# Optimization experiments

Measured on AMD Instinct MI355X. Metric: run time of the kernel, lower is better.

## Reference

```python
import jax, jax.numpy as jnp
import numpy as np

# iRPE config: ratio=1.9, method='euc', mode='ctx', shared_head=True, skip=1, rpe_on='k'
ALPHA, BETA, GAMMA = 1.9, 3.8, 15.2  # alpha=1*ratio, beta=2*ratio, gamma=8*ratio
NUM_HEADS = 12


def _rp_bucket_euc(height, width, skip):
    """Static relative-position bucket ids (Euclidean method, piecewise index).
    Returns (skip+L, skip+L) int array and num_buckets."""
    coords = np.stack(np.meshgrid(np.arange(height), np.arange(width), indexing='ij'), -1)
    coords = coords.reshape(-1, 2).astype(np.float64)  # (L, 2)
    diff = coords[:, None, :] - coords[None, :, :]      # (L, L, 2)
    dis = np.round(np.sqrt((diff ** 2).sum(-1)))        # (L, L), nonnegative
    # piecewise_index: identity for dis<=alpha, log-spaced (rounded, clipped at beta) beyond
    log_idx = np.minimum(
        np.round(ALPHA + np.log(np.maximum(dis, 1e-9) / ALPHA) / np.log(GAMMA / ALPHA) * (BETA - ALPHA)),
        BETA).astype(np.int64)
    bucket = np.where(dis <= ALPHA, np.round(dis).astype(np.int64), log_idx)
    bucket = bucket - bucket.min()
    nb = 2 * int(BETA) + 1  # 7
    if skip > 0:
        L = height * width
        full = np.full((skip + L, skip + L), nb, dtype=np.int64)  # extra bucket for cls token
        full[skip:, skip:] = bucket
        bucket, nb = full, nb + 1  # nb = 8
    return jnp.asarray(bucket), nb


def setup_inputs() -> dict:
    key = jax.random.key(0)
    ks = jax.random.split(key, 4)
    B, N, C = 8, 1025, 768  # 32x32 patches + 1 cls token
    hd = C // NUM_HEADS
    nb = 2 * int(BETA) + 1 + 1  # 8 buckets (incl. skip bucket)
    return {
        "x": jax.random.normal(ks[0], (B, N, C), jnp.float32),
        "qkv_w": jax.random.normal(ks[1], (3 * C, C), jnp.float32) * 0.02,
        "proj_w": jax.random.normal(ks[2], (C, C), jnp.float32) * 0.02,
        "proj_b": jnp.zeros((C,), jnp.float32),
        "rpe_w": jax.random.normal(ks[3], (hd, nb), jnp.float32) * 0.02,  # shared across heads
    }


def reference(x, qkv_w, proj_w, proj_b, rpe_w):
    B, N, C = x.shape
    H = NUM_HEADS
    hd = C // H
    scale = hd ** -0.5
    n_modalities = 1
    height = int((N // n_modalities) ** 0.5)        # 32 (mask is None path)
    skip = N - n_modalities * height * height       # 1 (cls token)
    rp_bucket, _ = _rp_bucket_euc(height, height, skip)  # (N, N) int, static

    qkv = (x @ qkv_w.T).reshape(B, N, 3, H, hd).transpose(2, 0, 3, 1, 4)  # (3,B,H,N,hd)
    q, k, v = qkv[0] * scale, qkv[1], qkv[2]
    attn = jnp.einsum('bhid,bhjd->bhij', q, k)
    # contextual RPE on keys (shared head): bias[b,h,i,j] = q[b,h,i,:] @ rpe_w[:, bucket[i,j]]
    lookup = jnp.einsum('bhid,dm->bhim', q, rpe_w)                      # (B,H,N,nb)
    bias = jnp.take_along_axis(lookup, rp_bucket[None, None, :, :], axis=3)  # (B,H,N,N)
    attn = jax.nn.softmax(attn + bias, axis=-1)
    out = jnp.einsum('bhij,bhjd->bhid', attn, v)
    out = out.transpose(0, 2, 1, 3).reshape(B, N, C)
    return out @ proj_w.T + proj_b
```

## Files before the change

kernel.cpp:

```cpp
#include <hip/hip_runtime.h>
#include <math.h>

#define B_    8
#define N_    1025
#define H_    12
#define HD_   64
#define C_    768
#define BH_   (B_*H_)
#define NTOK  (B_*N_)
#define SCALE 0.125f
#define NPAD  1092
#define NPADV 1088

#define QKV_ELEMS (BH_*N_*HD_)

#define XB_OFF_B     ((size_t)0)
#define WQKV_OFF_B   (XB_OFF_B + (size_t)NTOK*C_*2)
#define WPROJ_OFF_B  (WQKV_OFF_B + (size_t)3*C_*C_*2)
#define QB_OFF_B     (WPROJ_OFF_B + (size_t)C_*C_*2)
#define KB_OFF_B     (QB_OFF_B + (size_t)QKV_ELEMS*2)
#define AOB_OFF_B    (KB_OFF_B + (size_t)QKV_ELEMS*2)
#define VT_OFF_B     (AOB_OFF_B + (size_t)QKV_ELEMS*2)
#define BUCKET_OFF_B (VT_OFF_B + (size_t)BH_*HD_*NPADV*2)

typedef __attribute__((ext_vector_type(8))) short s8bf;
typedef __attribute__((ext_vector_type(8))) unsigned short u8s;
typedef __attribute__((ext_vector_type(4))) float v4f;
typedef unsigned short ushort_t;

#define GLOAD16(gp, lp) __builtin_amdgcn_global_load_lds( \
    (const __attribute__((address_space(1))) unsigned int*)(gp), \
    (__attribute__((address_space(3))) unsigned int*)(lp), 16, 0, 0)

#define SBAR() do { \
    __builtin_amdgcn_sched_barrier(0); \
    asm volatile("s_barrier" ::: "memory"); \
    __builtin_amdgcn_sched_barrier(0); \
} while (0)
#define VMW(N) do { \
    __builtin_amdgcn_sched_barrier(0); \
    asm volatile("s_waitcnt vmcnt(" #N ")" ::: "memory"); \
    __builtin_amdgcn_sched_barrier(0); \
} while (0)

__device__ __forceinline__ unsigned short f2bf(float x) {
    union { float f; unsigned u; } v; v.f = x;
    unsigned r = v.u + 0x7FFFu + ((v.u >> 16) & 1u);
    return (unsigned short)(r >> 16);
}
__device__ __forceinline__ unsigned packbf_hu(float lo, float hi) {
    union { float f; unsigned u; } a, b; a.f = lo; b.f = hi;
    return ((a.u + 0x8000u) >> 16) | ((b.u + 0x8000u) & 0xFFFF0000u);
}

__global__ void bucket_kernel(unsigned char* __restrict__ bucketT) {
    int tid = blockIdx.x * 256 + threadIdx.x;
    if (tid >= N_ * NPAD) return;
    unsigned ut = (unsigned)tid;
    int j = ut / (unsigned)NPAD, i = ut % (unsigned)NPAD;
    if (i >= N_) i = N_ - 1;
    int bk;
    if (i < 1 || j < 1) {
        bk = 7;
    } else {
        int pi = i - 1, pj = j - 1;
        int dy = (pi >> 5) - (pj >> 5);
        int dx = (pi & 31) - (pj & 31);
        int d2 = dy*dy + dx*dx;
        bk = (d2 == 0) ? 0 : ((d2 <= 2) ? 1 : ((d2 <= 12) ? 2 : 3));
    }
    bucketT[tid] = (unsigned char)bk;
}

__global__ __launch_bounds__(256) void cast_kernel(
        const float* __restrict__ x, const float* __restrict__ w1,
        const float* __restrict__ w2,
        ushort_t* __restrict__ xb, ushort_t* __restrict__ w1b,
        ushort_t* __restrict__ w2b) {
    const int NX = NTOK * C_ / 8, NW1 = 3 * C_ * C_ / 8, NW2 = C_ * C_ / 8;
    int g = blockIdx.x * 256 + threadIdx.x;
    const float* src; ushort_t* dst; int idx;
    if (g < NX)                 { src = x;  dst = xb;  idx = g; }
    else if (g < NX + NW1)      { src = w1; dst = w1b; idx = g - NX; }
    else if (g < NX + NW1 + NW2){ src = w2; dst = w2b; idx = g - NX - NW1; }
    else return;
    size_t off = (size_t)idx * 8;
    float4 a = *(const float4*)(src + off);
    float4 c = *(const float4*)(src + off + 4);
    __align__(16) ushort_t h[8] = {f2bf(a.x), f2bf(a.y), f2bf(a.z), f2bf(a.w),
                                   f2bf(c.x), f2bf(c.y), f2bf(c.z), f2bf(c.w)};
    *(u8s*)(dst + off) = *(u8s*)h;
}

__global__ __launch_bounds__(256) void qkv_kernel(
        const ushort_t* __restrict__ xb, const ushort_t* __restrict__ wb,
        ushort_t* __restrict__ qb, ushort_t* __restrict__ kb, ushort_t* __restrict__ vt) {
    __shared__ __align__(16) ushort_t As0[128*64];
    __shared__ __align__(16) ushort_t Bs0[128*64];
    __shared__ __align__(16) ushort_t As1[128*64];
    __shared__ __align__(16) ushort_t Bs1[128*64];
    const int L = blockIdx.x + blockIdx.y * 65;
    const int xcd = L & 7, idx = L >> 3;
    const int wg = (xcd < 2 ? xcd * 147 : 2 * 147 + (xcd - 2) * 146) + idx;
    const int m0 = (wg / 18) * 128, c0 = (wg % 18) * 128;
    const int t = threadIdx.x;
    const int w = t >> 6, lane = t & 63, lc = lane & 15, lq = lane >> 4;
    const int wm = (w >> 1) * 64, wn = (w & 1) * 64;
    const int srow8 = w * 32 + (lane >> 3);
    const int gsw8  = (((lane & 7) ^ (lane >> 3)) & 7) * 8;

    v4f acc[4][4];
#pragma unroll
    for (int mt = 0; mt < 4; mt++)
#pragma unroll
        for (int nt = 0; nt < 4; nt++) acc[mt][nt] = (v4f){0.f, 0.f, 0.f, 0.f};

    auto STAGE = [&](ushort_t* Ad, ushort_t* Bd, int k0) {
#pragma unroll
        for (int i = 0; i < 4; i++) {
            int row = srow8 + i * 8;
            int m = m0 + row; if (m > NTOK - 1) m = NTOK - 1;
            GLOAD16(xb + (size_t)m * C_ + k0 + gsw8,           &Ad[(w*32 + i*8) * 64]);
            GLOAD16(wb + (size_t)(c0 + row) * C_ + k0 + gsw8,  &Bd[(w*32 + i*8) * 64]);
        }
    };
    auto COMPUTE = [&](const ushort_t* A, const ushort_t* B) {
#pragma unroll
        for (int kk = 0; kk < 64; kk += 32) {
            s8bf af[4], bf[4];
#pragma unroll
            for (int mt = 0; mt < 4; mt++)
                af[mt] = *(const s8bf*)&A[(wm + mt*16 + lc) * 64 + ((((kk>>3) + lq) ^ (lc & 7)) * 8)];
#pragma unroll
            for (int nt = 0; nt < 4; nt++)
                bf[nt] = *(const s8bf*)&B[(wn + nt*16 + lc) * 64 + ((((kk>>3) + lq) ^ (lc & 7)) * 8)];
#pragma unroll
            for (int mt = 0; mt < 4; mt++)
#pragma unroll
                for (int nt = 0; nt < 4; nt++)
                    acc[mt][nt] = __builtin_amdgcn_mfma_f32_16x16x32_bf16(af[mt], bf[nt], acc[mt][nt], 0, 0, 0);
        }
    };

    STAGE(As0, Bs0, 0);
#pragma unroll
    for (int it = 0; it < 6; ++it) {
        const int k0 = it * 128;
        if (k0 + 64 < C_) {
            STAGE(As1, Bs1, k0 + 64);
            asm volatile("s_waitcnt vmcnt(8)" ::: "memory");
        } else {
            asm volatile("s_waitcnt vmcnt(0)" ::: "memory");
        }
        SBAR();
        COMPUTE(As0, Bs0);
        SBAR();
        if (k0 + 128 < C_) {
            STAGE(As0, Bs0, k0 + 128);
            asm volatile("s_waitcnt vmcnt(8)" ::: "memory");
        } else {
            asm volatile("s_waitcnt vmcnt(0)" ::: "memory");
        }
        SBAR();
        COMPUTE(As1, Bs1);
        if (it < 5) SBAR();
    }

#pragma unroll
    for (int mt = 0; mt < 4; mt++) {
#pragma unroll
        for (int r = 0; r < 4; r++) {
            int m = m0 + wm + mt*16 + lq*4 + r;
            if (m >= NTOK) continue;
            unsigned um = (unsigned)m;
            int b = um / (unsigned)N_, n = um % (unsigned)N_;
#pragma unroll
            for (int nt = 0; nt < 4; nt++) {
                int c = c0 + wn + nt*16 + lc;
                int comp = c / C_, rem = c % C_;
                int h = rem >> 6, d0 = rem & 63;
                float val = acc[mt][nt][r] * ((comp == 0) ? SCALE : 1.0f);
                if (comp == 2) {
                    vt[((size_t)((b*H_ + h)*HD_ + d0))*NPADV + n] = f2bf(val);
                } else {
                    ushort_t* dst = (comp == 0) ? qb : kb;
                    dst[((size_t)((b*H_ + h)*N_ + n))*HD_ + d0] = f2bf(val);
                }
            }
        }
    }
}

#define LUTS 9

__global__ __launch_bounds__(256) void attn_kernel(
        const ushort_t* __restrict__ qb, const ushort_t* __restrict__ kb,
        const ushort_t* __restrict__ vt, const float* __restrict__ rpe,
        const unsigned char* __restrict__ bucketT, ushort_t* __restrict__ ao) {
    __shared__ __align__(16) ushort_t Ks0[64*64];
    __shared__ __align__(16) ushort_t Vs0[64*64];
    __shared__ __align__(16) ushort_t Ks1[64*64];
    __shared__ __align__(16) ushort_t Vs1[64*64];
    __shared__ float lut[64*LUTS];

    const int bh = blockIdx.x, it0 = blockIdx.y;
    const int b  = bh / H_, hh = bh % H_;
    const int i0 = it0 * 64;
    const int t  = threadIdx.x;
    const int w  = t >> 6, lane = t & 63, lc = lane & 15, lq = lane >> 4;
    const int row_w = w * 16;
    const int rs = lc & 7;
    const int gA = ((lq ^ rs) & 7) * 8;
    const int gB = (((lq + 4) ^ rs) & 7) * 8;

    const ushort_t* qp = qb + (size_t)bh * N_ * HD_;
    const ushort_t* kp = kb + (size_t)bh * N_ * HD_;
    const ushort_t* vp = vt + (size_t)bh * HD_ * NPADV;

    {
        int row = t >> 2, g0 = (t & 3) * 2, qrs = row & 7;
        int gi = i0 + row;
        u8s h0 = (u8s)0, h1 = (u8s)0;
        if (gi < N_) {
            h0 = *(const u8s*)(qp + (size_t)gi * HD_ + g0*8);
            h1 = *(const u8s*)(qp + (size_t)gi * HD_ + g0*8 + 8);
        }
        *(u8s*)&Vs1[row*64 + ((g0 ^ qrs) * 8)]       = h0;
        *(u8s*)&Vs1[row*64 + (((g0+1) ^ qrs) * 8)]   = h1;
    }
    if (t < 64) {
        float4 r0 = *(const float4*)(rpe + t*8);
        float4 r1 = *(const float4*)(rpe + t*8 + 4);
        const int gr = t >> 3, go = t & 7;
        float vals[8] = {r0.x, r0.y, r0.z, r0.w, r1.x, r1.y, r1.z, r1.w};
#pragma unroll
        for (int m = 0; m < 8; m++)
            Ks1[m*64 + ((gr ^ (m & 7)) * 8) + go] = f2bf(vals[m]);
    } else if (t < 128) {
        int idx = t - 64;
        int m = 8 + (idx >> 3), g = idx & 7;
        *(u8s*)&Ks1[m*64 + ((g ^ (m & 7)) * 8)] = (u8s)0;
    }
    __syncthreads();

    s8bf qf0 = *(s8bf*)&Vs1[(row_w + lc)*64 + gA];
    s8bf qf1 = *(s8bf*)&Vs1[(row_w + lc)*64 + gB];

    {
        s8bf rf0 = *(s8bf*)&Ks1[lc*64 + gA];
        s8bf rf1 = *(s8bf*)&Ks1[lc*64 + gB];
        v4f la = (v4f){0.f, 0.f, 0.f, 0.f};
        la = __builtin_amdgcn_mfma_f32_16x16x32_bf16(qf0, rf0, la, 0, 0, 0);
        la = __builtin_amdgcn_mfma_f32_16x16x32_bf16(qf1, rf1, la, 0, 0, 0);
        if (lc < 8) {
#pragma unroll
            for (int r = 0; r < 4; r++)
                lut[(row_w + lq*4 + r)*LUTS + lc] = la[r];
        }
    }

    int myrow = i0 + row_w + lc; if (myrow > N_ - 1) myrow = N_ - 1;
    const unsigned char* bkrow = bucketT + (size_t)myrow * NPAD;
    const int lutbase = (row_w + lc) * LUTS;
    const int jb0 = 8*lq, jb1 = 8*lq + 4, jb2 = 8*lq + 32, jb3 = 8*lq + 36;
    unsigned bk4[4];

    auto STAGEA = [&](ushort_t* Kd, ushort_t* Vd, int jbase) {
#pragma unroll
        for (int i = 0; i < 2; i++) {
            int s = w*16 + i*8 + (lane >> 3);
            int jr = 32*(s>>5) + 8*((s>>2)&3) + 4*((s>>4)&1) + (s&3);
            int gj = jbase + jr; if (gj > N_ - 1) gj = N_ - 1;
            GLOAD16(kp + (size_t)gj * HD_ + (((lane&7) ^ (s&7)) * 8), &Kd[(w*16 + i*8)*64]);
        }
#pragma unroll
        for (int i = 0; i < 2; i++) {
            int d = w*16 + i*8 + (lane >> 3);
            GLOAD16(vp + (size_t)d * NPADV + jbase + (((lane&7) ^ (d&7)) * 8), &Vd[(w*16 + i*8)*64]);
        }
    };

    v4f o[4];
    float lsum = 0.f;
#pragma unroll
    for (int dt = 0; dt < 4; dt++) o[dt] = (v4f){0.f, 0.f, 0.f, 0.f};

    auto TILE = [&](const ushort_t* Kb, const ushort_t* Vb, int nextj, bool tail) {
        v4f acc[4];
#pragma unroll
        for (int t4 = 0; t4 < 4; t4++) acc[t4] = (v4f){0.f, 0.f, 0.f, 0.f};
#pragma unroll
        for (int t4 = 0; t4 < 4; t4++) {
            s8bf kf0 = *(const s8bf*)&Kb[(t4*16 + lc)*64 + gA];
            s8bf kf1 = *(const s8bf*)&Kb[(t4*16 + lc)*64 + gB];
            acc[t4] = __builtin_amdgcn_mfma_f32_16x16x32_bf16(kf0, qf0, acc[t4], 0, 0, 0);
            acc[t4] = __builtin_amdgcn_mfma_f32_16x16x32_bf16(kf1, qf1, acc[t4], 0, 0, 0);
        }
        unsigned pw[8];
        if (!tail) {
#pragma unroll
            for (int t4 = 0; t4 < 4; t4++) {
                int k0b = (bk4[t4]      ) & 0xFF; float p0 = __expf(acc[t4][0] + lut[lutbase + k0b]);
                int k1b = (bk4[t4] >>  8) & 0xFF; float p1 = __expf(acc[t4][1] + lut[lutbase + k1b]);
                int k2b = (bk4[t4] >> 16) & 0xFF; float p2 = __expf(acc[t4][2] + lut[lutbase + k2b]);
                int k3b = (bk4[t4] >> 24)       ; float p3 = __expf(acc[t4][3] + lut[lutbase + k3b]);
                lsum += (p0 + p1) + (p2 + p3);
                pw[t4*2]     = packbf_hu(p0, p1);
                pw[t4*2 + 1] = packbf_hu(p2, p3);
            }
        } else {
            const int jbs[4] = {jb0, jb1, jb2, jb3};
#pragma unroll
            for (int t4 = 0; t4 < 4; t4++) {
                float pv[4];
#pragma unroll
                for (int r = 0; r < 4; r++) {
                    int bk = (bk4[t4] >> (8*r)) & 0xFF;
                    float p = __expf(acc[t4][r] + lut[lutbase + bk]);
                    if ((jbs[t4] + r) > 0) p = 0.f;
                    lsum += p;
                    pv[r] = p;
                }
                pw[t4*2]     = packbf_hu(pv[0], pv[1]);
                pw[t4*2 + 1] = packbf_hu(pv[2], pv[3]);
            }
        }
        if (nextj >= 0) {
            bk4[0] = *(const unsigned*)(bkrow + nextj + jb0);
            bk4[1] = *(const unsigned*)(bkrow + nextj + jb1);
            bk4[2] = *(const unsigned*)(bkrow + nextj + jb2);
            bk4[3] = *(const unsigned*)(bkrow + nextj + jb3);
        }
        s8bf pf0 = *(s8bf*)&pw[0];
        s8bf pf1 = *(s8bf*)&pw[4];
#pragma unroll
        for (int dt = 0; dt < 4; dt++) {
            s8bf vf0 = *(const s8bf*)&Vb[(dt*16 + lc)*64 + gA];
            s8bf vf1 = *(const s8bf*)&Vb[(dt*16 + lc)*64 + gB];
            o[dt] = __builtin_amdgcn_mfma_f32_16x16x32_bf16(pf0, vf0, o[dt], 0, 0, 0);
            o[dt] = __builtin_amdgcn_mfma_f32_16x16x32_bf16(pf1, vf1, o[dt], 0, 0, 0);
        }
    };

    STAGEA(Ks0, Vs0, 0);
    bk4[0] = *(const unsigned*)(bkrow + jb0);
    bk4[1] = *(const unsigned*)(bkrow + jb1);
    bk4[2] = *(const unsigned*)(bkrow + jb2);
    bk4[3] = *(const unsigned*)(bkrow + jb3);
    SBAR();

    for (int it = 0; it < 8; ++it) {
        const int j0 = it * 128;
        STAGEA(Ks1, Vs1, j0 + 64);
        VMW(4);
        SBAR();
        TILE(Ks0, Vs0, j0 + 64, false);
        SBAR();
        STAGEA(Ks0, Vs0, j0 + 128);
        VMW(4);
        SBAR();
        TILE(Ks1, Vs1, j0 + 128, false);
        SBAR();
    }
    VMW(0);
    SBAR();
    TILE(Ks0, Vs0, -1, true);

    lsum += __shfl_xor(lsum, 16);
    lsum += __shfl_xor(lsum, 32);
    if (lq == 0) lut[(row_w + lc)*LUTS + 8] = lsum;
    __builtin_amdgcn_s_waitcnt(0);
#pragma unroll
    for (int r = 0; r < 4; r++) {
        int i = i0 + row_w + lq*4 + r;
        if (i < N_) {
            float inv = 1.0f / lut[(row_w + lq*4 + r)*LUTS + 8];
#pragma unroll
            for (int dt = 0; dt < 4; dt++)
                ao[((size_t)(b*N_ + i))*C_ + hh*HD_ + dt*16 + lc] = f2bf(o[dt][r] * inv);
        }
    }
}

__global__ __launch_bounds__(256) void proj_kernel(
        const ushort_t* __restrict__ ab, const ushort_t* __restrict__ wb,
        const float* __restrict__ bias, float* __restrict__ out) {
    __shared__ __align__(16) ushort_t As0[128*64];
    __shared__ __align__(16) ushort_t Bs0[128*64];
    __shared__ __align__(16) ushort_t As1[128*64];
    __shared__ __align__(16) ushort_t Bs1[128*64];
    const int L = blockIdx.x + blockIdx.y * 65;
    const int xcd = L & 7, idx = L >> 3;
    const int wg = (xcd < 6 ? xcd * 49 : 6 * 49 + (xcd - 6) * 48) + idx;
    const int m0 = (wg / 6) * 128, c0 = (wg % 6) * 128;
    const int t = threadIdx.x;
    const int w = t >> 6, lane = t & 63, lc = lane & 15, lq = lane >> 4;
    const int wm = (w >> 1) * 64, wn = (w & 1) * 64;
    const int srow8 = w * 32 + (lane >> 3);
    const int gsw8  = (((lane & 7) ^ (lane >> 3)) & 7) * 8;

    v4f acc[4][4];
#pragma unroll
    for (int mt = 0; mt < 4; mt++)
#pragma unroll
        for (int nt = 0; nt < 4; nt++) acc[mt][nt] = (v4f){0.f, 0.f, 0.f, 0.f};

    auto STAGE = [&](ushort_t* Ad, ushort_t* Bd, int k0) {
#pragma unroll
        for (int i = 0; i < 4; i++) {
            int row = srow8 + i * 8;
            int m = m0 + row; if (m > NTOK - 1) m = NTOK - 1;
            GLOAD16(ab + (size_t)m * C_ + k0 + gsw8,           &Ad[(w*32 + i*8) * 64]);
            GLOAD16(wb + (size_t)(c0 + row) * C_ + k0 + gsw8,  &Bd[(w*32 + i*8) * 64]);
        }
    };
    auto COMPUTE = [&](const ushort_t* A, const ushort_t* B) {
#pragma unroll
        for (int kk = 0; kk < 64; kk += 32) {
            s8bf af[4], bf[4];
#pragma unroll
            for (int mt = 0; mt < 4; mt++)
                af[mt] = *(const s8bf*)&A[(wm + mt*16 + lc) * 64 + ((((kk>>3) + lq) ^ (lc & 7)) * 8)];
#pragma unroll
            for (int nt = 0; nt < 4; nt++)
                bf[nt] = *(const s8bf*)&B[(wn + nt*16 + lc) * 64 + ((((kk>>3) + lq) ^ (lc & 7)) * 8)];
#pragma unroll
            for (int mt = 0; mt < 4; mt++)
#pragma unroll
                for (int nt = 0; nt < 4; nt++)
                    acc[mt][nt] = __builtin_amdgcn_mfma_f32_16x16x32_bf16(af[mt], bf[nt], acc[mt][nt], 0, 0, 0);
        }
    };

    STAGE(As0, Bs0, 0);
#pragma unroll
    for (int it = 0; it < 6; ++it) {
        const int k0 = it * 128;
        if (k0 + 64 < C_) {
            STAGE(As1, Bs1, k0 + 64);
            asm volatile("s_waitcnt vmcnt(8)" ::: "memory");
        } else {
            asm volatile("s_waitcnt vmcnt(0)" ::: "memory");
        }
        SBAR();
        COMPUTE(As0, Bs0);
        SBAR();
        if (k0 + 128 < C_) {
            STAGE(As0, Bs0, k0 + 128);
            asm volatile("s_waitcnt vmcnt(8)" ::: "memory");
        } else {
            asm volatile("s_waitcnt vmcnt(0)" ::: "memory");
        }
        SBAR();
        COMPUTE(As1, Bs1);
        if (it < 5) SBAR();
    }

    float pb[4];
#pragma unroll
    for (int nt = 0; nt < 4; nt++) pb[nt] = bias[c0 + wn + nt*16 + lc];
#pragma unroll
    for (int mt = 0; mt < 4; mt++) {
#pragma unroll
        for (int r = 0; r < 4; r++) {
            int m = m0 + wm + mt*16 + lq*4 + r;
            if (m >= NTOK) continue;
#pragma unroll
            for (int nt = 0; nt < 4; nt++) {
                int c = c0 + wn + nt*16 + lc;
                out[(size_t)m * C_ + c] = acc[mt][nt][r] + pb[nt];
            }
        }
    }
}

extern "C" void kernel_launch(void* const* d_in, const int* in_sizes, int n_in,
                              void* d_out, int out_size, void* d_ws, size_t ws_size,
                              hipStream_t stream) {
    const float* x      = (const float*)d_in[0];
    const float* qkv_w  = (const float*)d_in[1];
    const float* proj_w = (const float*)d_in[2];
    const float* proj_b = (const float*)d_in[3];
    const float* rpe_w  = (const float*)d_in[4];
    float* out = (float*)d_out;

    char* ws = (char*)d_ws;
    ushort_t* xb   = (ushort_t*)(ws + XB_OFF_B);
    ushort_t* wqkv = (ushort_t*)(ws + WQKV_OFF_B);
    ushort_t* wprj = (ushort_t*)(ws + WPROJ_OFF_B);
    ushort_t* qb   = (ushort_t*)(ws + QB_OFF_B);
    ushort_t* kb   = (ushort_t*)(ws + KB_OFF_B);
    ushort_t* aob  = (ushort_t*)(ws + AOB_OFF_B);
    ushort_t* vt   = (ushort_t*)(ws + VT_OFF_B);
    unsigned char* bucketT = (unsigned char*)(ws + BUCKET_OFF_B);

    const int ncast = (NTOK*C_ + 3*C_*C_ + C_*C_) / 8;
    bucket_kernel<<<dim3((N_*NPAD + 255)/256), 256, 0, stream>>>(bucketT);
    cast_kernel<<<dim3((ncast + 255)/256), 256, 0, stream>>>(x, qkv_w, proj_w, xb, wqkv, wprj);
    qkv_kernel<<<dim3(65, 18), 256, 0, stream>>>(xb, wqkv, qb, kb, vt);
    attn_kernel<<<dim3(96, 17), 256, 0, stream>>>(qb, kb, vt, rpe_w, bucketT, aob);
    proj_kernel<<<dim3(65, 6), 256, 0, stream>>>(aob, wprj, proj_b, out);
}
```

Before: 232.1 us.

## Process two 64-row query tiles per attention block to reuse K/V tiles

```diff
diff --git a/kernel.cpp b/kernel.cpp
--- a/kernel.cpp
+++ b/kernel.cpp
@@ -201,11 +201,11 @@
     __shared__ __align__(16) ushort_t Vs0[64*64];
     __shared__ __align__(16) ushort_t Ks1[64*64];
     __shared__ __align__(16) ushort_t Vs1[64*64];
-    __shared__ float lut[64*LUTS];
+    __shared__ float lut[128*LUTS];
 
     const int bh = blockIdx.x, it0 = blockIdx.y;
     const int b  = bh / H_, hh = bh % H_;
-    const int i0 = it0 * 64;
+    const int i0 = it0 * 128;
     const int t  = threadIdx.x;
     const int w  = t >> 6, lane = t & 63, lc = lane & 15, lq = lane >> 4;
     const int row_w = w * 16;
@@ -243,27 +243,48 @@
     }
     __syncthreads();
 
-    s8bf qf0 = *(s8bf*)&Vs1[(row_w + lc)*64 + gA];
-    s8bf qf1 = *(s8bf*)&Vs1[(row_w + lc)*64 + gB];
+    s8bf qfa0 = *(s8bf*)&Vs1[(row_w + lc)*64 + gA];
+    s8bf qfa1 = *(s8bf*)&Vs1[(row_w + lc)*64 + gB];
+    s8bf rf0 = *(s8bf*)&Ks1[lc*64 + gA];
+    s8bf rf1 = *(s8bf*)&Ks1[lc*64 + gB];
+    v4f la_a = (v4f){0.f, 0.f, 0.f, 0.f};
+    la_a = __builtin_amdgcn_mfma_f32_16x16x32_bf16(qfa0, rf0, la_a, 0, 0, 0);
+    la_a = __builtin_amdgcn_mfma_f32_16x16x32_bf16(qfa1, rf1, la_a, 0, 0, 0);
+    __syncthreads();
 
     {
-        s8bf rf0 = *(s8bf*)&Ks1[lc*64 + gA];
-        s8bf rf1 = *(s8bf*)&Ks1[lc*64 + gB];
-        v4f la = (v4f){0.f, 0.f, 0.f, 0.f};
-        la = __builtin_amdgcn_mfma_f32_16x16x32_bf16(qf0, rf0, la, 0, 0, 0);
-        la = __builtin_amdgcn_mfma_f32_16x16x32_bf16(qf1, rf1, la, 0, 0, 0);
-        if (lc < 8) {
-#pragma unroll
-            for (int r = 0; r < 4; r++)
-                lut[(row_w + lq*4 + r)*LUTS + lc] = la[r];
-        }
-    }
-
-    int myrow = i0 + row_w + lc; if (myrow > N_ - 1) myrow = N_ - 1;
-    const unsigned char* bkrow = bucketT + (size_t)myrow * NPAD;
-    const int lutbase = (row_w + lc) * LUTS;
+        int row = t >> 2, g0 = (t & 3) * 2, qrs = row & 7;
+        int gi = i0 + 64 + row;
+        u8s h0 = (u8s)0, h1 = (u8s)0;
+        if (gi < N_) {
+            h0 = *(const u8s*)(qp + (size_t)gi * HD_ + g0*8);
+            h1 = *(const u8s*)(qp + (size_t)gi * HD_ + g0*8 + 8);
+        }
+        *(u8s*)&Vs1[row*64 + ((g0 ^ qrs) * 8)]       = h0;
+        *(u8s*)&Vs1[row*64 + (((g0+1) ^ qrs) * 8)]   = h1;
+    }
+    __syncthreads();
+    s8bf qfb0 = *(s8bf*)&Vs1[(row_w + lc)*64 + gA];
+    s8bf qfb1 = *(s8bf*)&Vs1[(row_w + lc)*64 + gB];
+    v4f la_b = (v4f){0.f, 0.f, 0.f, 0.f};
+    la_b = __builtin_amdgcn_mfma_f32_16x16x32_bf16(qfb0, rf0, la_b, 0, 0, 0);
+    la_b = __builtin_amdgcn_mfma_f32_16x16x32_bf16(qfb1, rf1, la_b, 0, 0, 0);
+    if (lc < 8) {
+#pragma unroll
+        for (int r = 0; r < 4; r++) {
+            lut[(row_w + lq*4 + r)*LUTS + lc]        = la_a[r];
+            lut[(64 + row_w + lq*4 + r)*LUTS + lc]   = la_b[r];
+        }
+    }
+
+    int myrow_a = i0 + row_w + lc;       if (myrow_a > N_ - 1) myrow_a = N_ - 1;
+    int myrow_b = i0 + 64 + row_w + lc;  if (myrow_b > N_ - 1) myrow_b = N_ - 1;
+    const unsigned char* bkrow_a = bucketT + (size_t)myrow_a * NPAD;
+    const unsigned char* bkrow_b = bucketT + (size_t)myrow_b * NPAD;
+    const int lutbase_a = (row_w + lc) * LUTS;
+    const int lutbase_b = (64 + row_w + lc) * LUTS;
     const int jb0 = 8*lq, jb1 = 8*lq + 4, jb2 = 8*lq + 32, jb3 = 8*lq + 36;
-    unsigned bk4[4];
+    unsigned bka[4], bkb[4];
 
     auto STAGEA = [&](ushort_t* Kd, ushort_t* Vd, int jbase) {
 #pragma unroll
@@ -280,73 +301,101 @@
         }
     };
 
-    v4f o[4];
-    float lsum = 0.f;
-#pragma unroll
-    for (int dt = 0; dt < 4; dt++) o[dt] = (v4f){0.f, 0.f, 0.f, 0.f};
+    v4f oa[4], ob[4];
+    float lsa = 0.f, lsb = 0.f;
+#pragma unroll
+    for (int dt = 0; dt < 4; dt++) { oa[dt] = (v4f){0.f,0.f,0.f,0.f}; ob[dt] = (v4f){0.f,0.f,0.f,0.f}; }
 
     auto TILE = [&](const ushort_t* Kb, const ushort_t* Vb, int nextj, bool tail) {
-        v4f acc[4];
-#pragma unroll
-        for (int t4 = 0; t4 < 4; t4++) acc[t4] = (v4f){0.f, 0.f, 0.f, 0.f};
+        v4f aa[4], ab[4];
+#pragma unroll
+        for (int t4 = 0; t4 < 4; t4++) { aa[t4] = (v4f){0.f,0.f,0.f,0.f}; ab[t4] = (v4f){0.f,0.f,0.f,0.f}; }
 #pragma unroll
         for (int t4 = 0; t4 < 4; t4++) {
             s8bf kf0 = *(const s8bf*)&Kb[(t4*16 + lc)*64 + gA];
             s8bf kf1 = *(const s8bf*)&Kb[(t4*16 + lc)*64 + gB];
-            acc[t4] = __builtin_amdgcn_mfma_f32_16x16x32_bf16(kf0, qf0, acc[t4], 0, 0, 0);
-            acc[t4] = __builtin_amdgcn_mfma_f32_16x16x32_bf16(kf1, qf1, acc[t4], 0, 0, 0);
-        }
-        unsigned pw[8];
+            aa[t4] = __builtin_amdgcn_mfma_f32_16x16x32_bf16(kf0, qfa0, aa[t4], 0, 0, 0);
+            aa[t4] = __builtin_amdgcn_mfma_f32_16x16x32_bf16(kf1, qfa1, aa[t4], 0, 0, 0);
+            ab[t4] = __builtin_amdgcn_mfma_f32_16x16x32_bf16(kf0, qfb0, ab[t4], 0, 0, 0);
+            ab[t4] = __builtin_amdgcn_mfma_f32_16x16x32_bf16(kf1, qfb1, ab[t4], 0, 0, 0);
+        }
+        unsigned pwa[8], pwb[8];
         if (!tail) {
 #pragma unroll
             for (int t4 = 0; t4 < 4; t4++) {
-                int k0b = (bk4[t4]      ) & 0xFF; float p0 = __expf(acc[t4][0] + lut[lutbase + k0b]);
-                int k1b = (bk4[t4] >>  8) & 0xFF; float p1 = __expf(acc[t4][1] + lut[lutbase + k1b]);
-                int k2b = (bk4[t4] >> 16) & 0xFF; float p2 = __expf(acc[t4][2] + lut[lutbase + k2b]);
-                int k3b = (bk4[t4] >> 24)       ; float p3 = __expf(acc[t4][3] + lut[lutbase + k3b]);
-                lsum += (p0 + p1) + (p2 + p3);
-                pw[t4*2]     = packbf_hu(p0, p1);
-                pw[t4*2 + 1] = packbf_hu(p2, p3);
+                int k0b = (bka[t4]      ) & 0xFF; float p0 = __expf(aa[t4][0] + lut[lutbase_a + k0b]);
+                int k1b = (bka[t4] >>  8) & 0xFF; float p1 = __expf(aa[t4][1] + lut[lutbase_a + k1b]);
+                int k2b = (bka[t4] >> 16) & 0xFF; float p2 = __expf(aa[t4][2] + lut[lutbase_a + k2b]);
+                int k3b = (bka[t4] >> 24)       ; float p3 = __expf(aa[t4][3] + lut[lutbase_a + k3b]);
+                lsa += (p0 + p1) + (p2 + p3);
+                pwa[t4*2]     = packbf_hu(p0, p1);
+                pwa[t4*2 + 1] = packbf_hu(p2, p3);
+            }
+#pragma unroll
+            for (int t4 = 0; t4 < 4; t4++) {
+                int k0b = (bkb[t4]      ) & 0xFF; float p0 = __expf(ab[t4][0] + lut[lutbase_b + k0b]);
+                int k1b = (bkb[t4] >>  8) & 0xFF; float p1 = __expf(ab[t4][1] + lut[lutbase_b + k1b]);
+                int k2b = (bkb[t4] >> 16) & 0xFF; float p2 = __expf(ab[t4][2] + lut[lutbase_b + k2b]);
+                int k3b = (bkb[t4] >> 24)       ; float p3 = __expf(ab[t4][3] + lut[lutbase_b + k3b]);
+                lsb += (p0 + p1) + (p2 + p3);
+                pwb[t4*2]     = packbf_hu(p0, p1);
+                pwb[t4*2 + 1] = packbf_hu(p2, p3);
             }
         } else {
             const int jbs[4] = {jb0, jb1, jb2, jb3};
 #pragma unroll
             for (int t4 = 0; t4 < 4; t4++) {
-                float pv[4];
+                float pva[4], pvb[4];
 #pragma unroll
                 for (int r = 0; r < 4; r++) {
-                    int bk = (bk4[t4] >> (8*r)) & 0xFF;
-                    float p = __expf(acc[t4][r] + lut[lutbase + bk]);
-                    if ((jbs[t4] + r) > 0) p = 0.f;
-                    lsum += p;
-                    pv[r] = p;
+                    bool jv = (jbs[t4] + r) == 0;
+                    int bk_a = (bka[t4] >> (8*r)) & 0xFF;
+                    float pa = __expf(aa[t4][r] + lut[lutbase_a + bk_a]);
+                    if (!jv) pa = 0.f;
+                    lsa += pa; pva[r] = pa;
+                    int bk_b = (bkb[t4] >> (8*r)) & 0xFF;
+                    float pb2 = __expf(ab[t4][r] + lut[lutbase_b + bk_b]);
+                    if (!jv) pb2 = 0.f;
+                    lsb += pb2; pvb[r] = pb2;
                 }
-                pw[t4*2]     = packbf_hu(pv[0], pv[1]);
-                pw[t4*2 + 1] = packbf_hu(pv[2], pv[3]);
+                pwa[t4*2] = packbf_hu(pva[0], pva[1]); pwa[t4*2+1] = packbf_hu(pva[2], pva[3]);
+                pwb[t4*2] = packbf_hu(pvb[0], pvb[1]); pwb[t4*2+1] = packbf_hu(pvb[2], pvb[3]);
             }
         }
         if (nextj >= 0) {
-            bk4[0] = *(const unsigned*)(bkrow + nextj + jb0);
-            bk4[1] = *(const unsigned*)(bkrow + nextj + jb1);
-            bk4[2] = *(const unsigned*)(bkrow + nextj + jb2);
-            bk4[3] = *(const unsigned*)(bkrow + nextj + jb3);
-        }
-        s8bf pf0 = *(s8bf*)&pw[0];
-        s8bf pf1 = *(s8bf*)&pw[4];
+            bka[0] = *(const unsigned*)(bkrow_a + nextj + jb0);
+            bka[1] = *(const unsigned*)(bkrow_a + nextj + jb1);
+            bka[2] = *(const unsigned*)(bkrow_a + nextj + jb2);
+            bka[3] = *(const unsigned*)(bkrow_a + nextj + jb3);
+            bkb[0] = *(const unsigned*)(bkrow_b + nextj + jb0);
+            bkb[1] = *(const unsigned*)(bkrow_b + nextj + jb1);
+            bkb[2] = *(const unsigned*)(bkrow_b + nextj + jb2);
+            bkb[3] = *(const unsigned*)(bkrow_b + nextj + jb3);
+        }
+        s8bf pfa0 = *(s8bf*)&pwa[0];
+        s8bf pfa1 = *(s8bf*)&pwa[4];
+        s8bf pfb0 = *(s8bf*)&pwb[0];
+        s8bf pfb1 = *(s8bf*)&pwb[4];
 #pragma unroll
         for (int dt = 0; dt < 4; dt++) {
             s8bf vf0 = *(const s8bf*)&Vb[(dt*16 + lc)*64 + gA];
             s8bf vf1 = *(const s8bf*)&Vb[(dt*16 + lc)*64 + gB];
-            o[dt] = __builtin_amdgcn_mfma_f32_16x16x32_bf16(pf0, vf0, o[dt], 0, 0, 0);
-            o[dt] = __builtin_amdgcn_mfma_f32_16x16x32_bf16(pf1, vf1, o[dt], 0, 0, 0);
+            oa[dt] = __builtin_amdgcn_mfma_f32_16x16x32_bf16(pfa0, vf0, oa[dt], 0, 0, 0);
+            oa[dt] = __builtin_amdgcn_mfma_f32_16x16x32_bf16(pfa1, vf1, oa[dt], 0, 0, 0);
+            ob[dt] = __builtin_amdgcn_mfma_f32_16x16x32_bf16(pfb0, vf0, ob[dt], 0, 0, 0);
+            ob[dt] = __builtin_amdgcn_mfma_f32_16x16x32_bf16(pfb1, vf1, ob[dt], 0, 0, 0);
         }
     };
 
     STAGEA(Ks0, Vs0, 0);
-    bk4[0] = *(const unsigned*)(bkrow + jb0);
-    bk4[1] = *(const unsigned*)(bkrow + jb1);
-    bk4[2] = *(const unsigned*)(bkrow + jb2);
-    bk4[3] = *(const unsigned*)(bkrow + jb3);
+    bka[0] = *(const unsigned*)(bkrow_a + jb0);
+    bka[1] = *(const unsigned*)(bkrow_a + jb1);
+    bka[2] = *(const unsigned*)(bkrow_a + jb2);
+    bka[3] = *(const unsigned*)(bkrow_a + jb3);
+    bkb[0] = *(const unsigned*)(bkrow_b + jb0);
+    bkb[1] = *(const unsigned*)(bkrow_b + jb1);
+    bkb[2] = *(const unsigned*)(bkrow_b + jb2);
+    bkb[3] = *(const unsigned*)(bkrow_b + jb3);
     SBAR();
 
     for (int it = 0; it < 8; ++it) {
@@ -366,9 +415,14 @@
     SBAR();
     TILE(Ks0, Vs0, -1, true);
 
-    lsum += __shfl_xor(lsum, 16);
-    lsum += __shfl_xor(lsum, 32);
-    if (lq == 0) lut[(row_w + lc)*LUTS + 8] = lsum;
+    lsa += __shfl_xor(lsa, 16);
+    lsa += __shfl_xor(lsa, 32);
+    lsb += __shfl_xor(lsb, 16);
+    lsb += __shfl_xor(lsb, 32);
+    if (lq == 0) {
+        lut[(row_w + lc)*LUTS + 8]      = lsa;
+        lut[(64 + row_w + lc)*LUTS + 8] = lsb;
+    }
     __builtin_amdgcn_s_waitcnt(0);
 #pragma unroll
     for (int r = 0; r < 4; r++) {
@@ -377,7 +431,14 @@
             float inv = 1.0f / lut[(row_w + lq*4 + r)*LUTS + 8];
 #pragma unroll
             for (int dt = 0; dt < 4; dt++)
-                ao[((size_t)(b*N_ + i))*C_ + hh*HD_ + dt*16 + lc] = f2bf(o[dt][r] * inv);
+                ao[((size_t)(b*N_ + i))*C_ + hh*HD_ + dt*16 + lc] = f2bf(oa[dt][r] * inv);
+        }
+        int i2 = i0 + 64 + row_w + lq*4 + r;
+        if (i2 < N_) {
+            float inv = 1.0f / lut[(64 + row_w + lq*4 + r)*LUTS + 8];
+#pragma unroll
+            for (int dt = 0; dt < 4; dt++)
+                ao[((size_t)(b*N_ + i2))*C_ + hh*HD_ + dt*16 + lc] = f2bf(ob[dt][r] * inv);
         }
     }
 }
@@ -498,6 +559,6 @@
     bucket_kernel<<<dim3((N_*NPAD + 255)/256), 256, 0, stream>>>(bucketT);
     cast_kernel<<<dim3((ncast + 255)/256), 256, 0, stream>>>(x, qkv_w, proj_w, xb, wqkv, wprj);
     qkv_kernel<<<dim3(65, 18), 256, 0, stream>>>(xb, wqkv, qb, kb, vt);
-    attn_kernel<<<dim3(96, 17), 256, 0, stream>>>(qb, kb, vt, rpe_w, bucketT, aob);
+    attn_kernel<<<dim3(96, 9), 256, 0, stream>>>(qb, kb, vt, rpe_w, bucketT, aob);
     proj_kernel<<<dim3(65, 6), 256, 0, stream>>>(aob, wprj, proj_b, out);
 }
```

Result: no change. 235.8 us (+1.6%).

## Replace double-buffered K/V staging with single buffer in attention kernel

Applied to the files above, without the earlier changes.

```diff
diff --git a/kernel.cpp b/kernel.cpp
--- a/kernel.cpp
+++ b/kernel.cpp
@@ -197,10 +197,8 @@
         const ushort_t* __restrict__ qb, const ushort_t* __restrict__ kb,
         const ushort_t* __restrict__ vt, const float* __restrict__ rpe,
         const unsigned char* __restrict__ bucketT, ushort_t* __restrict__ ao) {
-    __shared__ __align__(16) ushort_t Ks0[64*64];
-    __shared__ __align__(16) ushort_t Vs0[64*64];
-    __shared__ __align__(16) ushort_t Ks1[64*64];
-    __shared__ __align__(16) ushort_t Vs1[64*64];
+    __shared__ __align__(16) ushort_t Ks[64*64];
+    __shared__ __align__(16) ushort_t Vs[64*64];
     __shared__ float lut[64*LUTS];
 
     const int bh = blockIdx.x, it0 = blockIdx.y;
@@ -225,8 +223,8 @@
             h0 = *(const u8s*)(qp + (size_t)gi * HD_ + g0*8);
             h1 = *(const u8s*)(qp + (size_t)gi * HD_ + g0*8 + 8);
         }
-        *(u8s*)&Vs1[row*64 + ((g0 ^ qrs) * 8)]       = h0;
-        *(u8s*)&Vs1[row*64 + (((g0+1) ^ qrs) * 8)]   = h1;
+        *(u8s*)&Vs[row*64 + ((g0 ^ qrs) * 8)]       = h0;
+        *(u8s*)&Vs[row*64 + (((g0+1) ^ qrs) * 8)]   = h1;
     }
     if (t < 64) {
         float4 r0 = *(const float4*)(rpe + t*8);
@@ -235,20 +233,20 @@
         float vals[8] = {r0.x, r0.y, r0.z, r0.w, r1.x, r1.y, r1.z, r1.w};
 #pragma unroll
         for (int m = 0; m < 8; m++)
-            Ks1[m*64 + ((gr ^ (m & 7)) * 8) + go] = f2bf(vals[m]);
+            Ks[m*64 + ((gr ^ (m & 7)) * 8) + go] = f2bf(vals[m]);
     } else if (t < 128) {
         int idx = t - 64;
         int m = 8 + (idx >> 3), g = idx & 7;
-        *(u8s*)&Ks1[m*64 + ((g ^ (m & 7)) * 8)] = (u8s)0;
+        *(u8s*)&Ks[m*64 + ((g ^ (m & 7)) * 8)] = (u8s)0;
     }
     __syncthreads();
 
-    s8bf qf0 = *(s8bf*)&Vs1[(row_w + lc)*64 + gA];
-    s8bf qf1 = *(s8bf*)&Vs1[(row_w + lc)*64 + gB];
+    s8bf qf0 = *(s8bf*)&Vs[(row_w + lc)*64 + gA];
+    s8bf qf1 = *(s8bf*)&Vs[(row_w + lc)*64 + gB];
 
     {
-        s8bf rf0 = *(s8bf*)&Ks1[lc*64 + gA];
-        s8bf rf1 = *(s8bf*)&Ks1[lc*64 + gB];
+        s8bf rf0 = *(s8bf*)&Ks[lc*64 + gA];
+        s8bf rf1 = *(s8bf*)&Ks[lc*64 + gB];
         v4f la = (v4f){0.f, 0.f, 0.f, 0.f};
         la = __builtin_amdgcn_mfma_f32_16x16x32_bf16(qf0, rf0, la, 0, 0, 0);
         la = __builtin_amdgcn_mfma_f32_16x16x32_bf16(qf1, rf1, la, 0, 0, 0);
@@ -264,19 +262,23 @@
     const int lutbase = (row_w + lc) * LUTS;
     const int jb0 = 8*lq, jb1 = 8*lq + 4, jb2 = 8*lq + 32, jb3 = 8*lq + 36;
     unsigned bk4[4];
-
-    auto STAGEA = [&](ushort_t* Kd, ushort_t* Vd, int jbase) {
+    bk4[0] = *(const unsigned*)(bkrow + jb0);
+    bk4[1] = *(const unsigned*)(bkrow + jb1);
+    bk4[2] = *(const unsigned*)(bkrow + jb2);
+    bk4[3] = *(const unsigned*)(bkrow + jb3);
+
+    auto STAGEA = [&](int jbase) {
 #pragma unroll
         for (int i = 0; i < 2; i++) {
             int s = w*16 + i*8 + (lane >> 3);
             int jr = 32*(s>>5) + 8*((s>>2)&3) + 4*((s>>4)&1) + (s&3);
             int gj = jbase + jr; if (gj > N_ - 1) gj = N_ - 1;
-            GLOAD16(kp + (size_t)gj * HD_ + (((lane&7) ^ (s&7)) * 8), &Kd[(w*16 + i*8)*64]);
+            GLOAD16(kp + (size_t)gj * HD_ + (((lane&7) ^ (s&7)) * 8), &Ks[(w*16 + i*8)*64]);
         }
 #pragma unroll
         for (int i = 0; i < 2; i++) {
             int d = w*16 + i*8 + (lane >> 3);
-            GLOAD16(vp + (size_t)d * NPADV + jbase + (((lane&7) ^ (d&7)) * 8), &Vd[(w*16 + i*8)*64]);
+            GLOAD16(vp + (size_t)d * NPADV + jbase + (((lane&7) ^ (d&7)) * 8), &Vs[(w*16 + i*8)*64]);
         }
     };
 
@@ -285,14 +287,14 @@
 #pragma unroll
     for (int dt = 0; dt < 4; dt++) o[dt] = (v4f){0.f, 0.f, 0.f, 0.f};
 
-    auto TILE = [&](const ushort_t* Kb, const ushort_t* Vb, int nextj, bool tail) {
+    auto TILE = [&](int nextj, bool tail) {
         v4f acc[4];
 #pragma unroll
         for (int t4 = 0; t4 < 4; t4++) acc[t4] = (v4f){0.f, 0.f, 0.f, 0.f};
 #pragma unroll
         for (int t4 = 0; t4 < 4; t4++) {
-            s8bf kf0 = *(const s8bf*)&Kb[(t4*16 + lc)*64 + gA];
-            s8bf kf1 = *(const s8bf*)&Kb[(t4*16 + lc)*64 + gB];
+            s8bf kf0 = *(const s8bf*)&Ks[(t4*16 + lc)*64 + gA];
+            s8bf kf1 = *(const s8bf*)&Ks[(t4*16 + lc)*64 + gB];
             acc[t4] = __builtin_amdgcn_mfma_f32_16x16x32_bf16(kf0, qf0, acc[t4], 0, 0, 0);
             acc[t4] = __builtin_amdgcn_mfma_f32_16x16x32_bf16(kf1, qf1, acc[t4], 0, 0, 0);
         }
@@ -335,36 +337,25 @@
         s8bf pf1 = *(s8bf*)&pw[4];
 #pragma unroll
         for (int dt = 0; dt < 4; dt++) {
-            s8bf vf0 = *(const s8bf*)&Vb[(dt*16 + lc)*64 + gA];
-            s8bf vf1 = *(const s8bf*)&Vb[(dt*16 + lc)*64 + gB];
+            s8bf vf0 = *(const s8bf*)&Vs[(dt*16 + lc)*64 + gA];
+            s8bf vf1 = *(const s8bf*)&Vs[(dt*16 + lc)*64 + gB];
             o[dt] = __builtin_amdgcn_mfma_f32_16x16x32_bf16(pf0, vf0, o[dt], 0, 0, 0);
             o[dt] = __builtin_amdgcn_mfma_f32_16x16x32_bf16(pf1, vf1, o[dt], 0, 0, 0);
         }
     };
 
-    STAGEA(Ks0, Vs0, 0);
-    bk4[0] = *(const unsigned*)(bkrow + jb0);
-    bk4[1] = *(const unsigned*)(bkrow + jb1);
-    bk4[2] = *(const unsigned*)(bkrow + jb2);
-    bk4[3] = *(const unsigned*)(bkrow + jb3);
+    for (int jt = 0; jt < 16; jt++) {
+        SBAR();
+        STAGEA(jt * 64);
+        VMW(0);
+        SBAR();
+        TILE(jt * 64 + 64, false);
+    }
     SBAR();
-
-    for (int it = 0; it < 8; ++it) {
-        const int j0 = it * 128;
-        STAGEA(Ks1, Vs1, j0 + 64);
-        VMW(4);
-        SBAR();
-        TILE(Ks0, Vs0, j0 + 64, false);
-        SBAR();
-        STAGEA(Ks0, Vs0, j0 + 128);
-        VMW(4);
-        SBAR();
-        TILE(Ks1, Vs1, j0 + 128, false);
-        SBAR();
-    }
+    STAGEA(1024);
     VMW(0);
     SBAR();
-    TILE(Ks0, Vs0, -1, true);
+    TILE(-1, true);
 
     lsum += __shfl_xor(lsum, 16);
     lsum += __shfl_xor(lsum, 32);
```

Result: no change. 227.7 us (-1.9%).
